# Performance work log

Measured on AMD Instinct MI355X. Metric: run time of the kernel, lower is better.

The kernel has to match this reference:

```python
import jax, jax.numpy as jnp
import numpy as np
import math

D, H, HKV = 1024, 16, 4
DH = D // H  # 64
B, T = 2, 2048


def _rope_tables(T, Dh):
    pos = jnp.arange(T, dtype=jnp.float32)
    inv_freq = 1.0 / (10000.0 ** (jnp.arange(0, Dh, 2, dtype=jnp.float32) / Dh))
    ang = pos[:, None] * inv_freq[None, :]                 # [T, Dh/2]
    ang = jnp.concatenate([ang, ang], axis=-1)             # [T, Dh]
    return jnp.cos(ang)[None, None], jnp.sin(ang)[None, None]  # [1,1,T,Dh]


def setup_inputs() -> dict:
    key = jax.random.key(0)
    kx, kq, kk, kv, ko = jax.random.split(key, 5)
    x = jax.random.normal(kx, (B, T, D), dtype=jnp.float32)
    s = 1.0 / math.sqrt(D)
    Wq = jax.random.normal(kq, (H * DH, D), dtype=jnp.float32) * s
    Wk = jax.random.normal(kk, (HKV * DH, D), dtype=jnp.float32) * s
    Wv = jax.random.normal(kv, (HKV * DH, D), dtype=jnp.float32) * s
    Wo = jax.random.normal(ko, (D, D), dtype=jnp.float32) * s
    rope_cos, rope_sin = _rope_tables(T, DH)
    # additive causal mask: 0 on/below diagonal, -1e9 above
    causal = jnp.triu(jnp.full((T, T), -1e9, dtype=jnp.float32), k=1)[None, None]
    return {"x": x, "rope_cos": rope_cos, "rope_sin": rope_sin,
            "attn_mask": causal, "Wq": Wq, "Wk": Wk, "Wv": Wv, "Wo": Wo}


def _apply_rope(t, cos, sin):
    # t: [B,h,T,Dh]; cos/sin broadcast [1,1,T,Dh]
    Dh = t.shape[-1]
    t1, t2 = t[..., :Dh // 2], t[..., Dh // 2:]
    t_rot = jnp.concatenate([-t2, t1], axis=-1)
    Tlen = t.shape[2]
    return t * cos[..., :Tlen, :] + t_rot * sin[..., :Tlen, :]


def reference(x, rope_cos, rope_sin, attn_mask, Wq, Wk, Wv, Wo):
    Bx, Tx, Dx = x.shape
    q = (x @ Wq.T).reshape(Bx, Tx, H, DH).transpose(0, 2, 1, 3)    # [B,H,T,Dh]
    k = (x @ Wk.T).reshape(Bx, Tx, HKV, DH).transpose(0, 2, 1, 3)  # [B,Hkv,T,Dh]
    v = (x @ Wv.T).reshape(Bx, Tx, HKV, DH).transpose(0, 2, 1, 3)
    q = _apply_rope(q, rope_cos, rope_sin)
    k = _apply_rope(k, rope_cos, rope_sin)
    rep = H // HKV
    k = jnp.repeat(k, rep, axis=1)  # repeat_interleave on head dim
    v = jnp.repeat(v, rep, axis=1)
    att = jnp.einsum('bhtd,bhsd->bhts', q, k) / math.sqrt(DH)
    att = att + attn_mask
    att = jax.nn.softmax(att, axis=-1)
    y = jnp.einsum('bhts,bhsd->bhtd', att, v)
    y = y.transpose(0, 2, 1, 3).reshape(Bx, Tx, Dx)
    return y @ Wo.T
```

## Files before the change

kernel.cpp:

```cpp
#include <hip/hip_runtime.h>


typedef short bf16x8 __attribute__((ext_vector_type(8)));
typedef float f32x4 __attribute__((ext_vector_type(4)));

__device__ __forceinline__ unsigned short f2bf(float f) {
  unsigned u = __float_as_uint(f);
  u += 0x7fffu + ((u >> 16) & 1u);
  return (unsigned short)(u >> 16);
}

__device__ __forceinline__ unsigned cvt_pk_bf16(float lo, float hi) {
  unsigned r;
  asm("v_cvt_pk_bf16_f32 %0, %1, %2" : "=v"(r) : "v"(lo), "v"(hi));
  return r;
}

__device__ __forceinline__ float fexp2(float x) {
#if __has_builtin(__builtin_amdgcn_exp2f)
  return __builtin_amdgcn_exp2f(x);
#else
  return __expf(x * 0.69314718056f);
#endif
}

__device__ __forceinline__ void load_lds16(const void* g, void* l) {
  __builtin_amdgcn_global_load_lds(
      (const __attribute__((address_space(1))) void*)g,
      (__attribute__((address_space(3))) void*)l, 16, 0, 0);
}

__global__ __launch_bounds__(256) void cvt_kernel(const float* __restrict__ src,
                                                  unsigned short* __restrict__ dst,
                                                  int n4) {
  int i = blockIdx.x * blockDim.x + threadIdx.x;
  if (i >= n4) return;
  float4 v = reinterpret_cast<const float4*>(src)[i];
  ushort4 o;
  o.x = f2bf(v.x); o.y = f2bf(v.y); o.z = f2bf(v.z); o.w = f2bf(v.w);
  reinterpret_cast<ushort4*>(dst)[i] = o;
}

__global__ __launch_bounds__(256) void cvt_w4(const float* __restrict__ Wq,
                                              const float* __restrict__ Wk,
                                              const float* __restrict__ Wv,
                                              const float* __restrict__ Wo,
                                              unsigned short* __restrict__ Wcat,
                                              unsigned short* __restrict__ Wob) {
  int i = blockIdx.x * blockDim.x + threadIdx.x;
  const float* src; unsigned short* dst; int off;
  if (i < 262144)      { src = Wq; dst = Wcat;           off = i; }
  else if (i < 327680) { src = Wk; dst = Wcat + 1048576; off = i - 262144; }
  else if (i < 393216) { src = Wv; dst = Wcat + 1310720; off = i - 327680; }
  else                 { src = Wo; dst = Wob;            off = i - 393216; }
  float4 v = reinterpret_cast<const float4*>(src)[off];
  ushort4 o;
  o.x = f2bf(v.x); o.y = f2bf(v.y); o.z = f2bf(v.z); o.w = f2bf(v.w);
  reinterpret_cast<ushort4*>(dst)[off] = o;
}

__global__ __launch_bounds__(256) void gemm_bt(const unsigned short* __restrict__ A,
                                               const unsigned short* __restrict__ B,
                                               float* __restrict__ C,
                                               int M, int N, int K) {
  __shared__ unsigned short As[128][32];
  __shared__ unsigned short Bs[128][32];
  const int tid  = threadIdx.x;
  const int lane = tid & 63, wave = tid >> 6;
  const int wr = wave >> 1, wc = wave & 1;
  const int m0 = blockIdx.y * 128, n0 = blockIdx.x * 128;
  const int fr = lane & 15, k8 = (lane >> 4) * 8;
  f32x4 acc[4][4] = {};
  for (int kt = 0; kt < K; kt += 32) {
    __syncthreads();
#pragma unroll
    for (int j = 0; j < 2; ++j) {
      const int cs  = (j*4 + wave);
      const int c   = cs*64 + lane;
      const int row = c >> 2, col = (c & 3) * 8;
      load_lds16(A + (size_t)(m0 + row)*K + kt + col, (char*)&As[0][0] + (size_t)cs*1024);
      load_lds16(B + (size_t)(n0 + row)*K + kt + col, (char*)&Bs[0][0] + (size_t)cs*1024);
    }
    __syncthreads();
    bf16x8 af[4], bf[4];
#pragma unroll
    for (int i = 0; i < 4; ++i) af[i] = *(const bf16x8*)&As[wr*64 + i*16 + fr][k8];
#pragma unroll
    for (int i = 0; i < 4; ++i) bf[i] = *(const bf16x8*)&Bs[wc*64 + i*16 + fr][k8];
#pragma unroll
    for (int mi = 0; mi < 4; ++mi)
#pragma unroll
      for (int ni = 0; ni < 4; ++ni)
        acc[mi][ni] = __builtin_amdgcn_mfma_f32_16x16x32_bf16(af[mi], bf[ni], acc[mi][ni], 0, 0, 0);
  }
#pragma unroll
  for (int mi = 0; mi < 4; ++mi)
#pragma unroll
    for (int ni = 0; ni < 4; ++ni)
#pragma unroll
      for (int j = 0; j < 4; ++j) {
        int row = m0 + wr*64 + mi*16 + (lane >> 4)*4 + j;
        int col = n0 + wc*64 + ni*16 + fr;
        C[(size_t)row * N + col] = acc[mi][ni][j];
      }
}

__global__ __launch_bounds__(256) void gemm_qkv_rope(const unsigned short* __restrict__ A,
                                                     const unsigned short* __restrict__ Bw,
                                                     const float* __restrict__ rc,
                                                     const float* __restrict__ rs,
                                                     unsigned short* __restrict__ Qb,
                                                     unsigned short* __restrict__ Kb,
                                                     unsigned short* __restrict__ Vb) {
  const int K = 1024;
  __shared__ unsigned short As[128][32];
  __shared__ unsigned short Bs[128][32];
  const int tid  = threadIdx.x;
  const int lane = tid & 63, wave = tid >> 6;
  const int wr = wave >> 1, wc = wave & 1;
  const int m0 = blockIdx.y * 128, n0 = blockIdx.x * 128;
  const int fr = lane & 15, k8 = (lane >> 4) * 8;
  f32x4 acc[4][4] = {};
  for (int kt = 0; kt < K; kt += 32) {
    __syncthreads();
#pragma unroll
    for (int j = 0; j < 2; ++j) {
      const int cs  = (j*4 + wave);
      const int c   = cs*64 + lane;
      const int row = c >> 2, col = (c & 3) * 8;
      load_lds16(A  + (size_t)(m0 + row)*K + kt + col, (char*)&As[0][0] + (size_t)cs*1024);
      load_lds16(Bw + (size_t)(n0 + row)*K + kt + col, (char*)&Bs[0][0] + (size_t)cs*1024);
    }
    __syncthreads();
    bf16x8 af[4], bf[4];
#pragma unroll
    for (int i = 0; i < 4; ++i) af[i] = *(const bf16x8*)&As[wr*64 + i*16 + fr][k8];
#pragma unroll
    for (int i = 0; i < 4; ++i) bf[i] = *(const bf16x8*)&Bs[wc*64 + i*16 + fr][k8];
#pragma unroll
    for (int mi = 0; mi < 4; ++mi)
#pragma unroll
      for (int ni = 0; ni < 4; ++ni)
        acc[mi][ni] = __builtin_amdgcn_mfma_f32_16x16x32_bf16(af[mi], bf[ni], acc[mi][ni], 0, 0, 0);
  }
  const int rg = lane >> 4;
  const float SCLQ = 0.125f * 1.44269504089f;
  const int colbase = n0 + wc*64;
#pragma unroll
  for (int mi = 0; mi < 4; ++mi) {
#pragma unroll
    for (int j = 0; j < 4; ++j) {
      const int m = m0 + wr*64 + mi*16 + rg*4 + j;
      const int b = m >> 11, t = m & 2047;
      if (colbase < 1280) {
        float vr[4];
#pragma unroll
        for (int ni = 0; ni < 4; ++ni) {
          const int d = ni*16 + fr;
          float cs = rc[t*64 + d], sn = rs[t*64 + d];
          float x = acc[mi][ni][j];
          float partner = acc[mi][ni ^ 2][j];
          float rot = (ni < 2) ? -partner : partner;
          vr[ni] = x * cs + rot * sn;
        }
        if (colbase < 1024) {
          const int h = colbase >> 6;
          size_t base = ((size_t)((b*16 + h)*2048 + t) << 6);
#pragma unroll
          for (int ni = 0; ni < 4; ++ni) Qb[base + ni*16 + fr] = f2bf(vr[ni] * SCLQ);
        } else {
          const int kh = (colbase - 1024) >> 6;
          size_t base = ((size_t)((b*4 + kh)*2048 + t) << 6);
#pragma unroll
          for (int ni = 0; ni < 4; ++ni) Kb[base + ni*16 + fr] = f2bf(vr[ni]);
        }
      } else {
        const int vh = (colbase - 1280) >> 6;
#pragma unroll
        for (int ni = 0; ni < 4; ++ni) {
          const int d = ni*16 + fr;
          Vb[((size_t)((b*4 + vh)*64 + d))*2048 + t] = f2bf(acc[mi][ni][j]);
        }
      }
    }
  }
}

__global__ __launch_bounds__(256) void attn_kernel(const unsigned short* __restrict__ Qb,
                                                   const unsigned short* __restrict__ Kb,
                                                   const unsigned short* __restrict__ Vb,
                                                   unsigned short* __restrict__ Yb) {
  __shared__ unsigned short Ks[2][64][72];
  __shared__ unsigned short Vt[2][64][72];
  __shared__ unsigned PpA[4][32][20];
  __shared__ unsigned PpB[4][32][20];
  const int p = blockIdx.x, bh = blockIdx.y;
  const int b = bh >> 4, h = bh & 15, kvh = h >> 2;
  const int qtA = 31 - p, qtB = p;
  const int nkv = qtA + 1;
  const int tid = threadIdx.x;
  const int wave = tid >> 6, lane = tid & 63;
  const int fr = lane & 15, g = lane >> 4, k8 = g * 8;
  const int srow = tid >> 3, scol = (tid & 7) * 8;
  const unsigned short* Kp = Kb + ((size_t)(b*4 + kvh)*2048) * 64;
  const unsigned short* Vp = Vb + ((size_t)(b*4 + kvh)*64) * 2048;
  const unsigned short* QpA = Qb + ((size_t)((b*16 + h)*2048 + qtA*64)) * 64;
  const unsigned short* QpB = Qb + ((size_t)((b*16 + h)*2048 + qtB*64)) * 64;
  bf16x8 qfA0 = *(const bf16x8*)(QpA + (wave*16 + fr)*64 + k8);
  bf16x8 qfA1 = *(const bf16x8*)(QpA + (wave*16 + fr)*64 + 32 + k8);
  bf16x8 qfB0 = *(const bf16x8*)(QpB + (wave*16 + fr)*64 + k8);
  bf16x8 qfB1 = *(const bf16x8*)(QpB + (wave*16 + fr)*64 + 32 + k8);
  float mA = -3.0e38f, lsA = 0.f, mB = -3.0e38f, lsB = 0.f;
  f32x4 accA[4] = {}, accB[4] = {};
  const int qgA = qtA*64 + wave*16 + fr;
  const int qgB = qtB*64 + wave*16 + fr;

  bf16x8 kreg[2], vreg[2];
#pragma unroll
  for (int j = 0; j < 2; ++j) {
    kreg[j] = *(const bf16x8*)(Kp + (size_t)(srow + j*32)*64 + scol);
    vreg[j] = *(const bf16x8*)(Vp + (size_t)(srow + j*32)*2048 + scol);
  }
#pragma unroll
  for (int j = 0; j < 2; ++j) {
    *(bf16x8*)&Ks[0][srow + j*32][scol] = kreg[j];
    *(bf16x8*)&Vt[0][srow + j*32][scol] = vreg[j];
  }
  __syncthreads();

  for (int kt = 0; kt < nkv; ++kt) {
    const int kv0 = kt * 64;
    const int cur = kt & 1;
    const bool actB = (kt <= qtB);
    const bool more = (kt + 1 < nkv);
    if (more) {
      const size_t nv0 = (size_t)(kt + 1) * 64;
#pragma unroll
      for (int j = 0; j < 2; ++j) {
        kreg[j] = *(const bf16x8*)(Kp + (nv0 + srow + j*32)*64 + scol);
        vreg[j] = *(const bf16x8*)(Vp + (size_t)(srow + j*32)*2048 + nv0 + scol);
      }
    }
    f32x4 sA[4] = {}, sB[4] = {};
    __builtin_amdgcn_s_setprio(1);
#pragma unroll
    for (int n = 0; n < 4; ++n) {
      bf16x8 kf0 = *(const bf16x8*)&Ks[cur][n*16 + fr][k8];
      sA[n] = __builtin_amdgcn_mfma_f32_16x16x32_bf16(kf0, qfA0, sA[n], 0, 0, 0);
      if (actB) sB[n] = __builtin_amdgcn_mfma_f32_16x16x32_bf16(kf0, qfB0, sB[n], 0, 0, 0);
      bf16x8 kf1 = *(const bf16x8*)&Ks[cur][n*16 + fr][32 + k8];
      sA[n] = __builtin_amdgcn_mfma_f32_16x16x32_bf16(kf1, qfA1, sA[n], 0, 0, 0);
      if (actB) sB[n] = __builtin_amdgcn_mfma_f32_16x16x32_bf16(kf1, qfB1, sB[n], 0, 0, 0);
    }
    __builtin_amdgcn_s_setprio(0);
    {
      float sv[4][4];
      if (kt == qtA) {
#pragma unroll
        for (int n = 0; n < 4; ++n)
#pragma unroll
          for (int r = 0; r < 4; ++r)
            sv[n][r] = (kv0 + n*16 + g*4 + r > qgA) ? -3.0e38f : sA[n][r];
      } else {
#pragma unroll
        for (int n = 0; n < 4; ++n)
#pragma unroll
          for (int r = 0; r < 4; ++r) sv[n][r] = sA[n][r];
      }
      float t4[4];
#pragma unroll
      for (int n = 0; n < 4; ++n)
        t4[n] = fmaxf(fmaxf(sv[n][0], sv[n][1]), fmaxf(sv[n][2], sv[n][3]));
      float tm = fmaxf(fmaxf(t4[0], t4[1]), fmaxf(t4[2], t4[3]));
      tm = fmaxf(tm, __shfl_xor(tm, 16));
      tm = fmaxf(tm, __shfl_xor(tm, 32));
      float mn = fmaxf(mA, tm);
      float al = fexp2(mA - mn);
      mA = mn;
      lsA *= al;
#pragma unroll
      for (int dt = 0; dt < 4; ++dt) accA[dt] *= al;
#pragma unroll
      for (int n = 0; n < 4; ++n)
#pragma unroll
        for (int r2 = 0; r2 < 2; ++r2) {
          float p0 = fexp2(sv[n][2*r2]   - mA);
          float p1 = fexp2(sv[n][2*r2+1] - mA);
          lsA += p0 + p1;
          PpA[wave][n*8 + g*2 + r2][fr] = cvt_pk_bf16(p0, p1);
        }
    }
    if (actB) {
      float sv[4][4];
      if (kt == qtB) {
#pragma unroll
        for (int n = 0; n < 4; ++n)
#pragma unroll
          for (int r = 0; r < 4; ++r)
            sv[n][r] = (kv0 + n*16 + g*4 + r > qgB) ? -3.0e38f : sB[n][r];
      } else {
#pragma unroll
        for (int n = 0; n < 4; ++n)
#pragma unroll
          for (int r = 0; r < 4; ++r) sv[n][r] = sB[n][r];
      }
      float t4[4];
#pragma unroll
      for (int n = 0; n < 4; ++n)
        t4[n] = fmaxf(fmaxf(sv[n][0], sv[n][1]), fmaxf(sv[n][2], sv[n][3]));
      float tm = fmaxf(fmaxf(t4[0], t4[1]), fmaxf(t4[2], t4[3]));
      tm = fmaxf(tm, __shfl_xor(tm, 16));
      tm = fmaxf(tm, __shfl_xor(tm, 32));
      float mn = fmaxf(mB, tm);
      float al = fexp2(mB - mn);
      mB = mn;
      lsB *= al;
#pragma unroll
      for (int dt = 0; dt < 4; ++dt) accB[dt] *= al;
#pragma unroll
      for (int n = 0; n < 4; ++n)
#pragma unroll
        for (int r2 = 0; r2 < 2; ++r2) {
          float p0 = fexp2(sv[n][2*r2]   - mB);
          float p1 = fexp2(sv[n][2*r2+1] - mB);
          lsB += p0 + p1;
          PpB[wave][n*8 + g*2 + r2][fr] = cvt_pk_bf16(p0, p1);
        }
    }
    __builtin_amdgcn_s_setprio(1);
#pragma unroll
    for (int c = 0; c < 2; ++c) {
      union { unsigned u[4]; bf16x8 v; } pa, pb;
#pragma unroll
      for (int i2 = 0; i2 < 4; ++i2) pa.u[i2] = PpA[wave][c*16 + g*4 + i2][fr];
      if (actB) {
#pragma unroll
        for (int i2 = 0; i2 < 4; ++i2) pb.u[i2] = PpB[wave][c*16 + g*4 + i2][fr];
      }
#pragma unroll
      for (int dt = 0; dt < 4; ++dt) {
        bf16x8 vf = *(const bf16x8*)&Vt[cur][dt*16 + fr][c*32 + k8];
        accA[dt] = __builtin_amdgcn_mfma_f32_16x16x32_bf16(vf, pa.v, accA[dt], 0, 0, 0);
        if (actB) accB[dt] = __builtin_amdgcn_mfma_f32_16x16x32_bf16(vf, pb.v, accB[dt], 0, 0, 0);
      }
    }
    __builtin_amdgcn_s_setprio(0);
    if (more) {
#pragma unroll
      for (int j = 0; j < 2; ++j) {
        *(bf16x8*)&Ks[cur ^ 1][srow + j*32][scol] = kreg[j];
        *(bf16x8*)&Vt[cur ^ 1][srow + j*32][scol] = vreg[j];
      }
      __syncthreads();
    }
  }
  {
    float ls = lsA;
    ls += __shfl_xor(ls, 16);
    ls += __shfl_xor(ls, 32);
    const float inv = 1.0f / ls;
    size_t base = ((size_t)(b*2048 + qgA) << 10) + h*64;
#pragma unroll
    for (int dt = 0; dt < 4; ++dt) {
      uint2 pk;
      pk.x = cvt_pk_bf16(accA[dt][0] * inv, accA[dt][1] * inv);
      pk.y = cvt_pk_bf16(accA[dt][2] * inv, accA[dt][3] * inv);
      *(uint2*)&Yb[base + dt*16 + g*4] = pk;
    }
  }
  {
    float ls = lsB;
    ls += __shfl_xor(ls, 16);
    ls += __shfl_xor(ls, 32);
    const float inv = 1.0f / ls;
    size_t base = ((size_t)(b*2048 + qgB) << 10) + h*64;
#pragma unroll
    for (int dt = 0; dt < 4; ++dt) {
      uint2 pk;
      pk.x = cvt_pk_bf16(accB[dt][0] * inv, accB[dt][1] * inv);
      pk.y = cvt_pk_bf16(accB[dt][2] * inv, accB[dt][3] * inv);
      *(uint2*)&Yb[base + dt*16 + g*4] = pk;
    }
  }
}

extern "C" void kernel_launch(void* const* d_in, const int* in_sizes, int n_in,
                              void* d_out, int out_size, void* d_ws, size_t ws_size,
                              hipStream_t stream) {
  const float* x  = (const float*)d_in[0];
  const float* rc = (const float*)d_in[1];
  const float* rs = (const float*)d_in[2];
  const float* Wq = (const float*)d_in[4];
  const float* Wk = (const float*)d_in[5];
  const float* Wv = (const float*)d_in[6];
  const float* Wo = (const float*)d_in[7];
  float* out = (float*)d_out;

  char* ws = (char*)d_ws;
  unsigned short* xb   = (unsigned short*)(ws);
  unsigned short* Wcat = (unsigned short*)(ws + 8388608);
  unsigned short* Wob  = (unsigned short*)(ws + 11534336);
  unsigned short* Qb   = (unsigned short*)(ws + 38797312);
  unsigned short* Kb   = (unsigned short*)(ws + 47185920);
  unsigned short* Vb   = (unsigned short*)(ws + 49283072);
  unsigned short* Yb   = (unsigned short*)(ws + 51380224);

  cvt_kernel<<<4096, 256, 0, stream>>>(x, xb, 1048576);
  cvt_w4<<<2560, 256, 0, stream>>>(Wq, Wk, Wv, Wo, Wcat, Wob);
  gemm_qkv_rope<<<dim3(12, 32), 256, 0, stream>>>(xb, Wcat, rc, rs, Qb, Kb, Vb);
  attn_kernel<<<dim3(16, 32), 256, 0, stream>>>(Qb, Kb, Vb, Yb);
  gemm_bt<<<dim3(8, 32), 256, 0, stream>>>(Yb, Wob, out, 4096, 1024, 1024);
}
```

Measured before the change: 135.0 us.

## Double-buffer LDS tiles in projection GEMMs to overlap loads with MFMA

Both the generic GEMM and the fused QKV+RoPE GEMM now keep two LDS buffers and issue the global-to-LDS loads for the next K tile before computing on the current one. This cuts one barrier per iteration and is meant to hide global load latency behind the MFMA work. It doubles LDS use per block, which may lower occupancy. There is also a possible race: the async LDS loads are only waited on at the trailing barrier, so correctness depends on that barrier draining the outstanding vmcnt.

Measured after the change: 134.8 us. About the same (-0.1%).

```diff
diff --git a/kernel.cpp b/kernel.cpp
--- a/kernel.cpp
+++ b/kernel.cpp
@@ -63,35 +63,51 @@
                                                const unsigned short* __restrict__ B,
                                                float* __restrict__ C,
                                                int M, int N, int K) {
-  __shared__ unsigned short As[128][32];
-  __shared__ unsigned short Bs[128][32];
+  __shared__ unsigned short As[2][128][32];
+  __shared__ unsigned short Bs[2][128][32];
   const int tid  = threadIdx.x;
   const int lane = tid & 63, wave = tid >> 6;
   const int wr = wave >> 1, wc = wave & 1;
   const int m0 = blockIdx.y * 128, n0 = blockIdx.x * 128;
   const int fr = lane & 15, k8 = (lane >> 4) * 8;
+  const int nT = K >> 5;
   f32x4 acc[4][4] = {};
-  for (int kt = 0; kt < K; kt += 32) {
-    __syncthreads();
-#pragma unroll
-    for (int j = 0; j < 2; ++j) {
-      const int cs  = (j*4 + wave);
-      const int c   = cs*64 + lane;
-      const int row = c >> 2, col = (c & 3) * 8;
-      load_lds16(A + (size_t)(m0 + row)*K + kt + col, (char*)&As[0][0] + (size_t)cs*1024);
-      load_lds16(B + (size_t)(n0 + row)*K + kt + col, (char*)&Bs[0][0] + (size_t)cs*1024);
-    }
-    __syncthreads();
+
+  const int scs0 = wave, scs1 = 4 + wave;
+#define GSTAGE(sel, kt)                                                          \
+  {                                                                              \
+    {                                                                            \
+      const int c = scs0*64 + lane, row = c >> 2, col = (c & 3) * 8;             \
+      load_lds16(A + (size_t)(m0 + row)*K + (kt) + col,                          \
+                 (char*)&As[sel][0][0] + (size_t)scs0*1024);                     \
+      load_lds16(B + (size_t)(n0 + row)*K + (kt) + col,                          \
+                 (char*)&Bs[sel][0][0] + (size_t)scs0*1024);                     \
+    }                                                                            \
+    {                                                                            \
+      const int c = scs1*64 + lane, row = c >> 2, col = (c & 3) * 8;             \
+      load_lds16(A + (size_t)(m0 + row)*K + (kt) + col,                          \
+                 (char*)&As[sel][0][0] + (size_t)scs1*1024);                     \
+      load_lds16(B + (size_t)(n0 + row)*K + (kt) + col,                          \
+                 (char*)&Bs[sel][0][0] + (size_t)scs1*1024);                     \
+    }                                                                            \
+  }
+
+  GSTAGE(0, 0);
+  __syncthreads();
+  for (int t = 0; t < nT; ++t) {
+    const int cur = t & 1;
+    if (t + 1 < nT) GSTAGE(cur ^ 1, (t + 1) * 32);
     bf16x8 af[4], bf[4];
 #pragma unroll
-    for (int i = 0; i < 4; ++i) af[i] = *(const bf16x8*)&As[wr*64 + i*16 + fr][k8];
-#pragma unroll
-    for (int i = 0; i < 4; ++i) bf[i] = *(const bf16x8*)&Bs[wc*64 + i*16 + fr][k8];
+    for (int i = 0; i < 4; ++i) af[i] = *(const bf16x8*)&As[cur][wr*64 + i*16 + fr][k8];
+#pragma unroll
+    for (int i = 0; i < 4; ++i) bf[i] = *(const bf16x8*)&Bs[cur][wc*64 + i*16 + fr][k8];
 #pragma unroll
     for (int mi = 0; mi < 4; ++mi)
 #pragma unroll
       for (int ni = 0; ni < 4; ++ni)
         acc[mi][ni] = __builtin_amdgcn_mfma_f32_16x16x32_bf16(af[mi], bf[ni], acc[mi][ni], 0, 0, 0);
+    __syncthreads();
   }
 #pragma unroll
   for (int mi = 0; mi < 4; ++mi)
@@ -113,35 +129,48 @@
                                                      unsigned short* __restrict__ Kb,
                                                      unsigned short* __restrict__ Vb) {
   const int K = 1024;
-  __shared__ unsigned short As[128][32];
-  __shared__ unsigned short Bs[128][32];
+  __shared__ unsigned short As[2][128][32];
+  __shared__ unsigned short Bs[2][128][32];
   const int tid  = threadIdx.x;
   const int lane = tid & 63, wave = tid >> 6;
   const int wr = wave >> 1, wc = wave & 1;
   const int m0 = blockIdx.y * 128, n0 = blockIdx.x * 128;
   const int fr = lane & 15, k8 = (lane >> 4) * 8;
   f32x4 acc[4][4] = {};
-  for (int kt = 0; kt < K; kt += 32) {
-    __syncthreads();
-#pragma unroll
-    for (int j = 0; j < 2; ++j) {
-      const int cs  = (j*4 + wave);
-      const int c   = cs*64 + lane;
-      const int row = c >> 2, col = (c & 3) * 8;
-      load_lds16(A  + (size_t)(m0 + row)*K + kt + col, (char*)&As[0][0] + (size_t)cs*1024);
-      load_lds16(Bw + (size_t)(n0 + row)*K + kt + col, (char*)&Bs[0][0] + (size_t)cs*1024);
-    }
-    __syncthreads();
+  const int scs0 = wave, scs1 = 4 + wave;
+#define QSTAGE(sel, kt)                                                          \
+  {                                                                              \
+    {                                                                            \
+      const int c = scs0*64 + lane, row = c >> 2, col = (c & 3) * 8;             \
+      load_lds16(A  + (size_t)(m0 + row)*K + (kt) + col,                         \
+                 (char*)&As[sel][0][0] + (size_t)scs0*1024);                     \
+      load_lds16(Bw + (size_t)(n0 + row)*K + (kt) + col,                         \
+                 (char*)&Bs[sel][0][0] + (size_t)scs0*1024);                     \
+    }                                                                            \
+    {                                                                            \
+      const int c = scs1*64 + lane, row = c >> 2, col = (c & 3) * 8;             \
+      load_lds16(A  + (size_t)(m0 + row)*K + (kt) + col,                         \
+                 (char*)&As[sel][0][0] + (size_t)scs1*1024);                     \
+      load_lds16(Bw + (size_t)(n0 + row)*K + (kt) + col,                         \
+                 (char*)&Bs[sel][0][0] + (size_t)scs1*1024);                     \
+    }                                                                            \
+  }
+  QSTAGE(0, 0);
+  __syncthreads();
+  for (int t = 0; t < 32; ++t) {
+    const int cur = t & 1;
+    if (t + 1 < 32) QSTAGE(cur ^ 1, (t + 1) * 32);
     bf16x8 af[4], bf[4];
 #pragma unroll
-    for (int i = 0; i < 4; ++i) af[i] = *(const bf16x8*)&As[wr*64 + i*16 + fr][k8];
-#pragma unroll
-    for (int i = 0; i < 4; ++i) bf[i] = *(const bf16x8*)&Bs[wc*64 + i*16 + fr][k8];
+    for (int i = 0; i < 4; ++i) af[i] = *(const bf16x8*)&As[cur][wr*64 + i*16 + fr][k8];
+#pragma unroll
+    for (int i = 0; i < 4; ++i) bf[i] = *(const bf16x8*)&Bs[cur][wc*64 + i*16 + fr][k8];
 #pragma unroll
     for (int mi = 0; mi < 4; ++mi)
 #pragma unroll
       for (int ni = 0; ni < 4; ++ni)
         acc[mi][ni] = __builtin_amdgcn_mfma_f32_16x16x32_bf16(af[mi], bf[ni], acc[mi][ni], 0, 0, 0);
+    __syncthreads();
   }
   const int rg = lane >> 4;
   const float SCLQ = 0.125f * 1.44269504089f;
```

## Double-buffer LDS in projection GEMMs and halve N tile to 64

Applied to the files above, without the earlier changes.

Both the QKV+RoPE GEMM and the output projection GEMM now double-buffer their LDS tiles, issuing the next k-slice's global-to-LDS loads before computing on the current one, with a single barrier per iteration. The N tile shrinks from 128 to 64, so each wave owns a 32x64 output slice and the grids double (24x32 and 16x32 blocks). The goal is to hide load latency and put more blocks on the GPU's CUs. The cost is less reuse of A per block and more redundant A traffic.

Result: faster. 124.9 us (-7.5%).

```diff
diff --git a/kernel.cpp b/kernel.cpp
--- a/kernel.cpp
+++ b/kernel.cpp
@@ -63,44 +63,52 @@
                                                const unsigned short* __restrict__ B,
                                                float* __restrict__ C,
                                                int M, int N, int K) {
-  __shared__ unsigned short As[128][32];
-  __shared__ unsigned short Bs[128][32];
+  __shared__ unsigned short As[2][128][32];
+  __shared__ unsigned short Bs[2][64][32];
   const int tid  = threadIdx.x;
   const int lane = tid & 63, wave = tid >> 6;
-  const int wr = wave >> 1, wc = wave & 1;
-  const int m0 = blockIdx.y * 128, n0 = blockIdx.x * 128;
+  const int m0 = blockIdx.y * 128, n0 = blockIdx.x * 64;
   const int fr = lane & 15, k8 = (lane >> 4) * 8;
-  f32x4 acc[4][4] = {};
-  for (int kt = 0; kt < K; kt += 32) {
-    __syncthreads();
-#pragma unroll
-    for (int j = 0; j < 2; ++j) {
-      const int cs  = (j*4 + wave);
-      const int c   = cs*64 + lane;
-      const int row = c >> 2, col = (c & 3) * 8;
-      load_lds16(A + (size_t)(m0 + row)*K + kt + col, (char*)&As[0][0] + (size_t)cs*1024);
-      load_lds16(B + (size_t)(n0 + row)*K + kt + col, (char*)&Bs[0][0] + (size_t)cs*1024);
-    }
-    __syncthreads();
-    bf16x8 af[4], bf[4];
-#pragma unroll
-    for (int i = 0; i < 4; ++i) af[i] = *(const bf16x8*)&As[wr*64 + i*16 + fr][k8];
-#pragma unroll
-    for (int i = 0; i < 4; ++i) bf[i] = *(const bf16x8*)&Bs[wc*64 + i*16 + fr][k8];
-#pragma unroll
-    for (int mi = 0; mi < 4; ++mi)
+  const int nT = K >> 5;
+  f32x4 acc[2][4] = {};
+  const int ca0 = wave, ca1 = 4 + wave;
+#define BT_STAGE(sel, kt)                                                        \
+  {                                                                              \
+    { const int c = ca0*64 + lane, row = c >> 2, col = (c & 3) * 8;              \
+      load_lds16(A + (size_t)(m0 + row)*K + (kt) + col,                          \
+                 (char*)&As[sel][0][0] + (size_t)ca0*1024); }                    \
+    { const int c = ca1*64 + lane, row = c >> 2, col = (c & 3) * 8;              \
+      load_lds16(A + (size_t)(m0 + row)*K + (kt) + col,                          \
+                 (char*)&As[sel][0][0] + (size_t)ca1*1024); }                    \
+    { const int c = ca0*64 + lane, row = c >> 2, col = (c & 3) * 8;              \
+      load_lds16(B + (size_t)(n0 + row)*K + (kt) + col,                          \
+                 (char*)&Bs[sel][0][0] + (size_t)ca0*1024); }                    \
+  }
+  BT_STAGE(0, 0);
+  __syncthreads();
+  for (int t = 0; t < nT; ++t) {
+    const int cur = t & 1;
+    if (t + 1 < nT) BT_STAGE(cur ^ 1, (t + 1) * 32);
+    bf16x8 af[2], bf[4];
+#pragma unroll
+    for (int i = 0; i < 2; ++i) af[i] = *(const bf16x8*)&As[cur][wave*32 + i*16 + fr][k8];
+#pragma unroll
+    for (int i = 0; i < 4; ++i) bf[i] = *(const bf16x8*)&Bs[cur][i*16 + fr][k8];
+#pragma unroll
+    for (int mi = 0; mi < 2; ++mi)
 #pragma unroll
       for (int ni = 0; ni < 4; ++ni)
         acc[mi][ni] = __builtin_amdgcn_mfma_f32_16x16x32_bf16(af[mi], bf[ni], acc[mi][ni], 0, 0, 0);
-  }
-#pragma unroll
-  for (int mi = 0; mi < 4; ++mi)
+    __syncthreads();
+  }
+#pragma unroll
+  for (int mi = 0; mi < 2; ++mi)
 #pragma unroll
     for (int ni = 0; ni < 4; ++ni)
 #pragma unroll
       for (int j = 0; j < 4; ++j) {
-        int row = m0 + wr*64 + mi*16 + (lane >> 4)*4 + j;
-        int col = n0 + wc*64 + ni*16 + fr;
+        int row = m0 + wave*32 + mi*16 + (lane >> 4)*4 + j;
+        int col = n0 + ni*16 + fr;
         C[(size_t)row * N + col] = acc[mi][ni][j];
       }
 }
@@ -113,44 +121,51 @@
                                                      unsigned short* __restrict__ Kb,
                                                      unsigned short* __restrict__ Vb) {
   const int K = 1024;
-  __shared__ unsigned short As[128][32];
-  __shared__ unsigned short Bs[128][32];
+  __shared__ unsigned short As[2][128][32];
+  __shared__ unsigned short Bs[2][64][32];
   const int tid  = threadIdx.x;
   const int lane = tid & 63, wave = tid >> 6;
-  const int wr = wave >> 1, wc = wave & 1;
-  const int m0 = blockIdx.y * 128, n0 = blockIdx.x * 128;
+  const int m0 = blockIdx.y * 128, n0 = blockIdx.x * 64;
   const int fr = lane & 15, k8 = (lane >> 4) * 8;
-  f32x4 acc[4][4] = {};
-  for (int kt = 0; kt < K; kt += 32) {
-    __syncthreads();
-#pragma unroll
-    for (int j = 0; j < 2; ++j) {
-      const int cs  = (j*4 + wave);
-      const int c   = cs*64 + lane;
-      const int row = c >> 2, col = (c & 3) * 8;
-      load_lds16(A  + (size_t)(m0 + row)*K + kt + col, (char*)&As[0][0] + (size_t)cs*1024);
-      load_lds16(Bw + (size_t)(n0 + row)*K + kt + col, (char*)&Bs[0][0] + (size_t)cs*1024);
-    }
-    __syncthreads();
-    bf16x8 af[4], bf[4];
-#pragma unroll
-    for (int i = 0; i < 4; ++i) af[i] = *(const bf16x8*)&As[wr*64 + i*16 + fr][k8];
-#pragma unroll
-    for (int i = 0; i < 4; ++i) bf[i] = *(const bf16x8*)&Bs[wc*64 + i*16 + fr][k8];
-#pragma unroll
-    for (int mi = 0; mi < 4; ++mi)
+  f32x4 acc[2][4] = {};
+  const int ca0 = wave, ca1 = 4 + wave;
+#define QK_STAGE(sel, kt)                                                        \
+  {                                                                              \
+    { const int c = ca0*64 + lane, row = c >> 2, col = (c & 3) * 8;              \
+      load_lds16(A + (size_t)(m0 + row)*K + (kt) + col,                          \
+                 (char*)&As[sel][0][0] + (size_t)ca0*1024); }                    \
+    { const int c = ca1*64 + lane, row = c >> 2, col = (c & 3) * 8;              \
+      load_lds16(A + (size_t)(m0 + row)*K + (kt) + col,                          \
+                 (char*)&As[sel][0][0] + (size_t)ca1*1024); }                    \
+    { const int c = ca0*64 + lane, row = c >> 2, col = (c & 3) * 8;              \
+      load_lds16(Bw + (size_t)(n0 + row)*K + (kt) + col,                         \
+                 (char*)&Bs[sel][0][0] + (size_t)ca0*1024); }                    \
+  }
+  QK_STAGE(0, 0);
+  __syncthreads();
+  for (int t = 0; t < 32; ++t) {
+    const int cur = t & 1;
+    if (t + 1 < 32) QK_STAGE(cur ^ 1, (t + 1) * 32);
+    bf16x8 af[2], bf[4];
+#pragma unroll
+    for (int i = 0; i < 2; ++i) af[i] = *(const bf16x8*)&As[cur][wave*32 + i*16 + fr][k8];
+#pragma unroll
+    for (int i = 0; i < 4; ++i) bf[i] = *(const bf16x8*)&Bs[cur][i*16 + fr][k8];
+#pragma unroll
+    for (int mi = 0; mi < 2; ++mi)
 #pragma unroll
       for (int ni = 0; ni < 4; ++ni)
         acc[mi][ni] = __builtin_amdgcn_mfma_f32_16x16x32_bf16(af[mi], bf[ni], acc[mi][ni], 0, 0, 0);
+    __syncthreads();
   }
   const int rg = lane >> 4;
   const float SCLQ = 0.125f * 1.44269504089f;
-  const int colbase = n0 + wc*64;
-#pragma unroll
-  for (int mi = 0; mi < 4; ++mi) {
+  const int colbase = n0;
+#pragma unroll
+  for (int mi = 0; mi < 2; ++mi) {
 #pragma unroll
     for (int j = 0; j < 4; ++j) {
-      const int m = m0 + wr*64 + mi*16 + rg*4 + j;
+      const int m = m0 + wave*32 + mi*16 + rg*4 + j;
       const int b = m >> 11, t = m & 2047;
       if (colbase < 1280) {
         float vr[4];
@@ -407,7 +422,7 @@
 
   cvt_kernel<<<4096, 256, 0, stream>>>(x, xb, 1048576);
   cvt_w4<<<2560, 256, 0, stream>>>(Wq, Wk, Wv, Wo, Wcat, Wob);
-  gemm_qkv_rope<<<dim3(12, 32), 256, 0, stream>>>(xb, Wcat, rc, rs, Qb, Kb, Vb);
+  gemm_qkv_rope<<<dim3(24, 32), 256, 0, stream>>>(xb, Wcat, rc, rs, Qb, Kb, Vb);
   attn_kernel<<<dim3(16, 32), 256, 0, stream>>>(Qb, Kb, Vb, Yb);
-  gemm_bt<<<dim3(8, 32), 256, 0, stream>>>(Yb, Wob, out, 4096, 1024, 1024);
-}
+  gemm_bt<<<dim3(16, 32), 256, 0, stream>>>(Yb, Wob, out, 4096, 1024, 1024);
+}
```
